# Optimization experiments

Hardware: AMD Instinct MI355X
Metric: run time of the kernel (lower is better)

## Reference

```python
import jax, jax.numpy as jnp
import numpy as np

NE, NR = 200000, 500
D, TRI_H, TET_H = 128, 256, 256
NTRI, NTET = 500000, 200000
B = 8192
E_ET, E_TT, E_ETT = 1500000, 800000, 800000


def _mean_aggregate(src_idx, dst_idx, src, num_dst):
    # scatter-add of gathered messages, then divide by per-dst counts (0 -> 0)
    agg = jax.ops.segment_sum(src[src_idx], dst_idx, num_segments=num_dst)
    cnt = jax.ops.segment_sum(jnp.ones(src_idx.shape[0], dtype=src.dtype), dst_idx, num_segments=num_dst)
    return jnp.where((cnt > 0)[:, None], agg / jnp.maximum(cnt, 1.0)[:, None], 0.0)


def _layernorm(x, w, b, eps=1e-5):
    mu = jnp.mean(x, axis=-1, keepdims=True)
    var = jnp.mean((x - mu) ** 2, axis=-1, keepdims=True)
    return (x - mu) / jnp.sqrt(var + eps) * w + b


def setup_inputs():
    key = jax.random.key(0)
    ks = jax.random.split(key, 24)
    def xav(k, fan_out, fan_in):
        a = np.sqrt(6.0 / (fan_in + fan_out))
        return jax.random.uniform(k, (fan_out, fan_in), jnp.float32, -a, a)
    inp = {
        'entity_emb': xav(ks[0], NE, D),
        'relation_emb': xav(ks[1], NR, D),
        'g2_w1': xav(ks[2], TRI_H, D), 'g2_b1': jnp.zeros((TRI_H,), jnp.float32),
        'g2_w2': xav(ks[3], TRI_H, TRI_H), 'g2_b2': jnp.zeros((TRI_H,), jnp.float32),
        'g3_w1': xav(ks[4], TET_H, TRI_H), 'g3_b1': jnp.zeros((TET_H,), jnp.float32),
        'g3_w2': xav(ks[5], TET_H, TET_H), 'g3_b2': jnp.zeros((TET_H,), jnp.float32),
        'te_w': xav(ks[6], D, TET_H), 'te_b': jnp.zeros((D,), jnp.float32),
        'ln_w': jnp.ones((D,), jnp.float32), 'ln_b': jnp.zeros((D,), jnp.float32),
        'fusion_alpha': jnp.zeros((2,), jnp.float32),
        'gamma': jnp.array([12.0], jnp.float32),
        'triples': jax.random.randint(ks[7], (B, 3), 0, NR, jnp.int64 if jax.config.jax_enable_x64 else jnp.int32),
        'et_index': jax.random.randint(ks[8], (2, E_ET), 0, NE, jnp.int32),
        'tt_index': jax.random.randint(ks[9], (2, E_TT), 0, NTET, jnp.int32),
        'ent_tet_index': jax.random.randint(ks[10], (2, E_ETT), 0, NTET, jnp.int32),
        'num_triangles': NTRI,
        'num_tetras': NTET,
    }
    return inp


def reference(entity_emb, relation_emb, g2_w1, g2_b1, g2_w2, g2_b2,
              g3_w1, g3_b1, g3_w2, g3_b2, te_w, te_b, ln_w, ln_b,
              fusion_alpha, gamma, triples, et_index, tt_index,
              ent_tet_index, num_triangles, num_tetras):
    # gnn2: entity -> triangle  (segment-mean then Linear -> GELU -> Linear)
    tri_agg = _mean_aggregate(et_index[0], et_index[1], entity_emb, num_triangles)
    tri = jax.nn.gelu(tri_agg @ g2_w1.T + g2_b1, approximate=False) @ g2_w2.T + g2_b2
    # gnn3: triangle -> tetra
    tet_agg = _mean_aggregate(tt_index[0], tt_index[1], tri, num_tetras)
    tet = jax.nn.gelu(tet_agg @ g3_w1.T + g3_b1, approximate=False) @ g3_w2.T + g3_b2
    # project tetra -> entity dim, then tetra -> entity mean-aggregate (swapped index rows)
    tet_proj = tet @ te_w.T + te_b
    v_topo = _mean_aggregate(ent_tet_index[1], ent_tet_index[0], tet_proj, entity_emb.shape[0])
    v_topo = _layernorm(v_topo, ln_w, ln_b)
    # learned fusion
    w = jax.nn.softmax(fusion_alpha)
    V = w[0] * entity_emb + w[1] * v_topo
    # TransE scoring: gamma - ||V[h] + R[r] - V[t]||_2
    h, r, t = triples[:, 0], triples[:, 1], triples[:, 2]
    diff = V[h] + relation_emb[r] - V[t]
    return gamma[0] - jnp.sqrt(jnp.sum(diff * diff, axis=-1))
```

## Files before the change

kernel.cpp:

```cpp
#include <hip/hip_runtime.h>
#include <cmath>

#define NE_     200000
#define NR_     500
#define D_      128
#define TRIH_   256
#define TETH_   256
#define NTRI_   500000
#define NTET_   200000
#define B_      8192
#define EET_    1500000
#define ETT_    800000
#define EETT_   800000

#define CAP_V   2048
#define CAP_TP  8192
#define CAP_TRI 12288

#define LCAP_ET  131072
#define LCAP_TT  32768
#define LCAP_ETT 16384

#define COARSEN 8
#define CHUNK   (256 * COARSEN)

#define NBC_V   ((NE_   + CHUNK - 1) / CHUNK)
#define NBC_TP  ((NTET_ + CHUNK - 1) / CHUNK)
#define NBC_TRI ((NTRI_ + CHUNK - 1) / CHUNK)
#define NBF_ET  ((EET_  + CHUNK - 1) / CHUNK)
#define NBF_TT  ((ETT_  + CHUNK - 1) / CHUNK)
#define NBF_ETT ((EETT_ + CHUNK - 1) / CHUNK)
#define MARKB   1024

#define WB_G2W1 0
#define WB_G2W2 32768
#define WB_G3W1 98304
#define WB_G3W2 163840
#define WB_TE   229376


typedef float f32x4 __attribute__((ext_vector_type(4)));
typedef short s16x8 __attribute__((ext_vector_type(8)));

__device__ __forceinline__ float gelu_exact(float v) {
    return 0.5f * v * (1.0f + erff(v * 0.70710678118654752f));
}

__device__ __forceinline__ unsigned short f2bf(float f) {
    unsigned int u = __float_as_uint(f);
    unsigned int r = (u + 0x7fffu + ((u >> 16) & 1u)) >> 16;
    return (unsigned short)r;
}

__device__ __forceinline__ int wave_rank_emit(bool pred, int* lcnt, int lane) {
    unsigned long long mask = __ballot(pred);
    int rank = __popcll(mask & ((1ull << lane) - 1ull));
    int total = __popcll(mask);
    int wb = 0;
    if (lane == 0 && total) wb = atomicAdd(lcnt, total);
    wb = __shfl(wb, 0, 64);
    return pred ? (wb + rank) : -1;
}


__global__ void k_init(int* __restrict__ id_v, int* __restrict__ id_tp,
                       int* __restrict__ id_tri, int* __restrict__ ctr,
                       const float* __restrict__ w1, const float* __restrict__ w2,
                       const float* __restrict__ w3, const float* __restrict__ w4,
                       const float* __restrict__ w5, unsigned short* __restrict__ wb,
                       int* __restrict__ deg_tri, int* __restrict__ deg_tp,
                       int* __restrict__ deg_v) {
    int i = blockIdx.x * blockDim.x + threadIdx.x;
    int st = gridDim.x * blockDim.x;
    for (int x = i; x < NE_; x += st) id_v[x] = -1;
    for (int x = i; x < NTET_; x += st) id_tp[x] = -1;
    for (int x = i; x < NTRI_; x += st) id_tri[x] = -1;
    if (i < 16) ctr[i] = 0;
    for (int x = i; x < 262144; x += st) {
        float f;
        if (x < 32768)       f = w1[x];
        else if (x < 98304)  f = w2[x - 32768];
        else if (x < 163840) f = w3[x - 98304];
        else if (x < 229376) f = w4[x - 163840];
        else                 f = w5[x - 229376];
        wb[x] = f2bf(f);
    }
    for (int x = i; x < CAP_TRI; x += st) deg_tri[x] = 0;
    for (int x = i; x < CAP_TP; x += st) deg_tp[x] = 0;
    for (int x = i; x < CAP_V; x += st) deg_v[x] = 0;
}


__global__ void k_mark_v(const int* __restrict__ triples, int* __restrict__ id_v) {
    int b = blockIdx.x * blockDim.x + threadIdx.x;
    if (b >= B_) return;
    id_v[triples[b * 3 + 0]] = -2;
    id_v[triples[b * 3 + 2]] = -2;
}

__global__ void k_mark_tp(const int* __restrict__ ett, const int* __restrict__ id_v,
                          int* __restrict__ id_tp) {
    int i = blockIdx.x * blockDim.x + threadIdx.x;
    int st = gridDim.x * blockDim.x;
    for (int e = i; e < EETT_; e += st)
        if (id_v[ett[e]] != -1) id_tp[ett[EETT_ + e]] = -2;
}


__device__ void do_compact(int* __restrict__ arr, int n, int* __restrict__ g, int cap,
                           int bid, int* lcnt, int* lbase) {
    if (threadIdx.x == 0) *lcnt = 0;
    __syncthreads();
    const int lane = threadIdx.x & 63;
    const int base = bid * CHUNK;
    int pos[COARSEN];
#pragma unroll
    for (int u = 0; u < COARSEN; ++u) {
        int e = base + u * 256 + threadIdx.x;
        bool pred = (e < n) && (arr[e] == -2);
        pos[u] = wave_rank_emit(pred, lcnt, lane);
    }
    __syncthreads();
    if (threadIdx.x == 0) *lbase = *lcnt ? atomicAdd(g, *lcnt) : 0;
    __syncthreads();
    const int b0 = *lbase;
#pragma unroll
    for (int u = 0; u < COARSEN; ++u) {
        if (pos[u] >= 0) {
            int e = base + u * 256 + threadIdx.x;
            int idx = b0 + pos[u];
            arr[e] = (idx < cap) ? idx : -1;
        }
    }
}

__device__ void do_filter(const int* __restrict__ e0, const int* __restrict__ e1,
                          const int* __restrict__ map0, const int* __restrict__ map1,
                          int n, int2* __restrict__ list, int* __restrict__ nctr, int lcap,
                          int* __restrict__ deg, int bid, int* lcnt, int* lbase) {
    if (threadIdx.x == 0) *lcnt = 0;
    __syncthreads();
    const int lane = threadIdx.x & 63;
    const int base = bid * CHUNK;
    int pos[COARSEN]; int2 val[COARSEN];
#pragma unroll
    for (int u = 0; u < COARSEN; ++u) {
        int e = base + u * 256 + threadIdx.x;
        bool pred = false;
        int m1 = -1, src = -1;
        if (e < n) {
            m1 = map1[e1[e]];
            if (m1 >= 0) {
                src = map0 ? map0[e0[e]] : e0[e];
                pred = (src >= 0);
            }
        }
        pos[u] = wave_rank_emit(pred, lcnt, lane);
        if (pred) { val[u] = make_int2(src, m1); atomicAdd(&deg[m1], 1); }
    }
    __syncthreads();
    if (threadIdx.x == 0) *lbase = *lcnt ? atomicAdd(nctr, *lcnt) : 0;
    __syncthreads();
    const int b0 = *lbase;
#pragma unroll
    for (int u = 0; u < COARSEN; ++u)
        if (pos[u] >= 0 && b0 + pos[u] < lcap) list[b0 + pos[u]] = val[u];
}

__launch_bounds__(256)
__global__ void k_p4(const int* __restrict__ tt, int* __restrict__ id_v,
                     int* __restrict__ id_tp, int* __restrict__ id_tri,
                     int* __restrict__ ctr) {
    __shared__ int lcnt, lbase;
    int bid = blockIdx.x;
    if (bid < NBC_V) { do_compact(id_v, NE_, &ctr[0], CAP_V, bid, &lcnt, &lbase); return; }
    bid -= NBC_V;
    if (bid < NBC_TP) { do_compact(id_tp, NTET_, &ctr[1], CAP_TP, bid, &lcnt, &lbase); return; }
    bid -= NBC_TP;
    int i = bid * 256 + threadIdx.x;
    int st = MARKB * 256;
    for (int e = i; e < ETT_; e += st)
        if (id_tp[tt[ETT_ + e]] != -1) id_tri[tt[e]] = -2;
}

__launch_bounds__(256)
__global__ void k_p5(int* __restrict__ id_tri, const int* __restrict__ ett,
                     const int* __restrict__ id_v, const int* __restrict__ id_tp,
                     int2* __restrict__ list_ett, int* __restrict__ deg_v,
                     int* __restrict__ ctr) {
    __shared__ int lcnt, lbase;
    int bid = blockIdx.x;
    if (bid < NBC_TRI) { do_compact(id_tri, NTRI_, &ctr[2], CAP_TRI, bid, &lcnt, &lbase); return; }
    bid -= NBC_TRI;
    do_filter(ett + EETT_, ett, id_tp, id_v, EETT_, list_ett, &ctr[5], LCAP_ETT,
              deg_v, bid, &lcnt, &lbase);
}

__launch_bounds__(256)
__global__ void k_p6(const int* __restrict__ et, const int* __restrict__ tt,
                     const int* __restrict__ id_tri, const int* __restrict__ id_tp,
                     int2* __restrict__ list_et, int2* __restrict__ list_tt,
                     int* __restrict__ deg_tri, int* __restrict__ deg_tp,
                     int* __restrict__ ctr) {
    __shared__ int lcnt, lbase;
    int bid = blockIdx.x;
    if (bid < NBF_ET) {
        do_filter(et, et + EET_, nullptr, id_tri, EET_, list_et, &ctr[3], LCAP_ET,
                  deg_tri, bid, &lcnt, &lbase);
        return;
    }
    bid -= NBF_ET;
    do_filter(tt, tt + ETT_, id_tri, id_tp, ETT_, list_tt, &ctr[4], LCAP_TT,
              deg_tp, bid, &lcnt, &lbase);
}


__device__ void scan_level(const int* __restrict__ deg, int* __restrict__ start,
                           int* __restrict__ cur, int n) {
    __shared__ int wsum[16];
    const int tid = threadIdx.x;
    const int per = (n + 1023) >> 10;
    const int base = tid * per;
    int s = 0;
    for (int k = 0; k < per; ++k) { int i = base + k; if (i < n) s += deg[i]; }
    const int lane = tid & 63, wid = tid >> 6;
    int v = s;
#pragma unroll
    for (int o = 1; o < 64; o <<= 1) { int t = __shfl_up(v, o, 64); if (lane >= o) v += t; }
    if (lane == 63) wsum[wid] = v;
    __syncthreads();
    if (tid < 16) {
        int w = wsum[tid];
#pragma unroll
        for (int o = 1; o < 16; o <<= 1) { int t = __shfl_up(w, o, 64); if (tid >= o) w += t; }
        wsum[tid] = w;
    }
    __syncthreads();
    int run = v - s + (wid > 0 ? wsum[wid - 1] : 0);
    for (int k = 0; k < per; ++k) {
        int i = base + k;
        if (i < n) { start[i] = run; cur[i] = run; run += deg[i]; }
    }
    if (tid == 0) start[n] = wsum[15];
}

__global__ void k_scan(const int* __restrict__ deg_tri, int* __restrict__ st_tri, int* __restrict__ cu_tri,
                       const int* __restrict__ deg_tp, int* __restrict__ st_tp, int* __restrict__ cu_tp,
                       const int* __restrict__ deg_v, int* __restrict__ st_v, int* __restrict__ cu_v) {
    if (blockIdx.x == 0)      scan_level(deg_tri, st_tri, cu_tri, CAP_TRI);
    else if (blockIdx.x == 1) scan_level(deg_tp, st_tp, cu_tp, CAP_TP);
    else                      scan_level(deg_v, st_v, cu_v, CAP_V);
}

__global__ void k_bucket(const int* __restrict__ ctr,
                         const int2* __restrict__ le, int* __restrict__ cu_tri, int* __restrict__ be,
                         const int2* __restrict__ lt, int* __restrict__ cu_tp, int* __restrict__ btk,
                         const int2* __restrict__ lv, int* __restrict__ cu_v, int* __restrict__ bv) {
    int i = blockIdx.x * blockDim.x + threadIdx.x;
    int st = gridDim.x * blockDim.x;
    int n0 = min(ctr[3], LCAP_ET);
    for (int e = i; e < n0; e += st) {
        int2 p = le[e];
        int slot = atomicAdd(&cu_tri[p.y], 1);
        if (slot < LCAP_ET) be[slot] = p.x;
    }
    int n1 = min(ctr[4], LCAP_TT);
    for (int e = i; e < n1; e += st) {
        int2 p = lt[e];
        int slot = atomicAdd(&cu_tp[p.y], 1);
        if (slot < LCAP_TT) btk[slot] = p.x;
    }
    int n2 = min(ctr[5], LCAP_ETT);
    for (int e = i; e < n2; e += st) {
        int2 p = lv[e];
        int slot = atomicAdd(&cu_v[p.y], 1);
        if (slot < LCAP_ETT) bv[slot] = p.x;
    }
}


__global__ void k_gather_tri(const int* __restrict__ ctr, const int* __restrict__ st,
                             const int* __restrict__ bidx, const float* __restrict__ emb,
                             float* __restrict__ tri_agg) {
    const int c = min(ctr[2], CAP_TRI);
    const int lane = threadIdx.x & 63;
    int row = (blockIdx.x * blockDim.x + threadIdx.x) >> 6;
    const int nw = (gridDim.x * blockDim.x) >> 6;
    for (; row < c; row += nw) {
        int s0 = min(st[row], LCAP_ET), s1 = min(st[row + 1], LCAP_ET);
        float2 acc = make_float2(0.f, 0.f);
        for (int e = s0; e < s1; ++e) {
            unsigned si = (unsigned)bidx[e];
            if (si < NE_) {
                float2 v = ((const float2*)(emb + (size_t)si * 128))[lane];
                acc.x += v.x; acc.y += v.y;
            }
        }
        float inv = (s1 > s0) ? 1.f / (float)(s1 - s0) : 0.f;
        acc.x *= inv; acc.y *= inv;
        ((float2*)(tri_agg + (size_t)row * 128))[lane] = acc;
    }
}


template<int KU>
__device__ __forceinline__ f32x4 tile_mma(const unsigned short* xs, const unsigned short* ws,
                                          int ra, int rb, int fo) {
    f32x4 acc = {0.f, 0.f, 0.f, 0.f};
    const uint4* pa = (const uint4*)xs + ra * KU;
    const uint4* pb = (const uint4*)ws + rb * KU;
    const int sa = ra & 7, sb = rb & 7;
#pragma unroll
    for (int kk = 0; kk < KU / 4; ++kk) {
        s16x8 a = *(const s16x8*)&pa[(kk * 4 + fo) ^ sa];
        s16x8 b = *(const s16x8*)&pb[(kk * 4 + fo) ^ sb];
        acc = __builtin_amdgcn_mfma_f32_16x16x32_bf16(a, b, acc, 0, 0, 0);
    }
    return acc;
}


template<int K, int ACT>
__launch_bounds__(256)
__global__ void k_gemm(const int* __restrict__ ctrp, int ctr_idx, int cap,
                       const float* __restrict__ A,
                       const unsigned short* __restrict__ Wb, const float* __restrict__ bias,
                       float* __restrict__ C, int N) {
    constexpr int KU = K / 8;
    __shared__ __align__(16) unsigned short xs[32 * KU * 8];
    __shared__ __align__(16) unsigned short ws[32 * KU * 8];
    const int c = min(ctrp[ctr_idx], cap);
    const int row0 = blockIdx.x * 32;
    if (row0 >= c) return;
    const int tid = threadIdx.x;
    const int gc0 = blockIdx.y * 32;
#pragma unroll
    for (int it = 0; it < KU / 8; ++it) {
        int u = tid + it * 256;
        int r = u / KU, ku = u % KU;
        int gr = row0 + r;
        s16x8 v;
        if (gr < c) {
            const float* src = &A[(size_t)gr * K + ku * 8];
#pragma unroll
            for (int q = 0; q < 8; ++q) v[q] = (short)f2bf(src[q]);
        } else {
#pragma unroll
            for (int q = 0; q < 8; ++q) v[q] = 0;
        }
        *(s16x8*)&xs[(r * KU + (ku ^ (r & 7))) * 8] = v;
    }
#pragma unroll
    for (int it = 0; it < KU / 8; ++it) {
        int u = tid + it * 256;
        int r = u / KU, ku = u % KU;
        *(uint4*)&ws[(r * KU + (ku ^ (r & 7))) * 8] =
            *(const uint4*)&Wb[(size_t)(gc0 + r) * K + ku * 8];
    }
    __syncthreads();
    const int w = tid >> 6, l = tid & 63;
    const int wr = (w >> 1) * 16, wc = (w & 1) * 16;
    const int fr = l & 15, fo = l >> 4;
    f32x4 acc = tile_mma<KU>(xs, ws, wr + fr, wc + fr, fo);
    const int gcol = gc0 + wc + fr;
    const float bb = bias[gcol];
#pragma unroll
    for (int j = 0; j < 4; ++j) {
        int grow = row0 + wr + fo * 4 + j;
        if (grow < c) {
            float v = acc[j] + bb;
            if (ACT == 1) v = gelu_exact(v);
            C[(size_t)grow * N + gcol] = v;
        }
    }
}


__launch_bounds__(256)
__global__ void k_tet1(const int* __restrict__ ctrp, const int* __restrict__ st,
                       const int* __restrict__ bidx, const float* __restrict__ tri_c,
                       const unsigned short* __restrict__ wb, const float* __restrict__ b1,
                       float* __restrict__ h_tet) {
    __shared__ __align__(16) unsigned short xs[32 * 32 * 8];
    __shared__ __align__(16) unsigned short ws[32 * 32 * 8];
    const int c = min(ctrp[1], CAP_TP);
    const int row0 = blockIdx.x * 32;
    if (row0 >= c) return;
    const int tid = threadIdx.x, lane = tid & 63, wv = tid >> 6;
    for (int rr = wv * 8; rr < wv * 8 + 8; ++rr) {
        int row = row0 + rr;
        float a0 = 0.f, a1 = 0.f, a2 = 0.f, a3 = 0.f;
        int d = 0;
        if (row < c) {
            int s0 = min(st[row], LCAP_TT), s1 = min(st[row + 1], LCAP_TT);
            d = s1 - s0;
            for (int e = s0; e < s1; ++e) {
                unsigned si = (unsigned)bidx[e];
                if (si < CAP_TRI) {
                    float4 v = ((const float4*)(tri_c + (size_t)si * 256))[lane];
                    a0 += v.x; a1 += v.y; a2 += v.z; a3 += v.w;
                }
            }
        }
        float inv = (d > 0) ? 1.f / (float)d : 0.f;
        unsigned lo = (unsigned)f2bf(a0 * inv) | ((unsigned)f2bf(a1 * inv) << 16);
        unsigned hi = (unsigned)f2bf(a2 * inv) | ((unsigned)f2bf(a3 * inv) << 16);
        int col0 = lane * 4;
        int ku = col0 >> 3, off = col0 & 7;
        *(uint2*)&xs[((rr << 5) + (ku ^ (rr & 7))) * 8 + off] = make_uint2(lo, hi);
    }
    const int oc = blockIdx.y;
#pragma unroll
    for (int it = 0; it < 4; ++it) {
        int u = tid + it * 256, r = u >> 5, ku = u & 31;
        *(uint4*)&ws[((r << 5) + (ku ^ (r & 7))) * 8] =
            *(const uint4*)&wb[WB_G3W1 + (size_t)(oc * 32 + r) * 256 + ku * 8];
    }
    __syncthreads();
    const int w = tid >> 6;
    const int wr = (w >> 1) * 16, wc = (w & 1) * 16;
    const int fr = lane & 15, fo = lane >> 4;
    f32x4 acc = tile_mma<32>(xs, ws, wr + fr, wc + fr, fo);
    int col = oc * 32 + wc + fr;
    float bb = b1[col];
#pragma unroll
    for (int j = 0; j < 4; ++j) {
        int grow = row0 + wr + fo * 4 + j;
        if (grow < c) h_tet[(size_t)grow * 256 + col] = gelu_exact(acc[j] + bb);
    }
}


__global__ void k_final(const float* __restrict__ emb, const float* __restrict__ rel,
                        const float* __restrict__ tet_proj, const int* __restrict__ st_v,
                        const int* __restrict__ b_ett, const int* __restrict__ id_v,
                        const float* __restrict__ lnw, const float* __restrict__ lnb,
                        const float* __restrict__ alpha, const float* __restrict__ gamma,
                        const int* __restrict__ triples, float* __restrict__ out) {
    const int lane = threadIdx.x & 63;
    const int b = blockIdx.x * 4 + (threadIdx.x >> 6);
    if (b >= B_) return;
    float a0 = alpha[0], a1 = alpha[1];
    float m = fmaxf(a0, a1);
    float e0 = expf(a0 - m), e1 = expf(a1 - m);
    float w0 = e0 / (e0 + e1), w1 = e1 / (e0 + e1);
    int h = triples[b * 3 + 0];
    int r = triples[b * 3 + 1];
    int t = triples[b * 3 + 2];
    int jh = id_v[h]; jh = (jh >= 0 && jh < CAP_V) ? jh : 0;
    int jt = id_v[t]; jt = (jt >= 0 && jt < CAP_V) ? jt : 0;

    float2 xh = make_float2(0.f, 0.f), xt = make_float2(0.f, 0.f);
    {
        int s0 = min(st_v[jh], LCAP_ETT), s1 = min(st_v[jh + 1], LCAP_ETT);
        for (int e = s0; e < s1; ++e) {
            unsigned si = (unsigned)b_ett[e];
            if (si < CAP_TP) {
                float2 v = ((const float2*)(tet_proj + (size_t)si * 128))[lane];
                xh.x += v.x; xh.y += v.y;
            }
        }
        float inv = (s1 > s0) ? 1.f / (float)(s1 - s0) : 0.f;
        xh.x *= inv; xh.y *= inv;
    }
    {
        int s0 = min(st_v[jt], LCAP_ETT), s1 = min(st_v[jt + 1], LCAP_ETT);
        for (int e = s0; e < s1; ++e) {
            unsigned si = (unsigned)b_ett[e];
            if (si < CAP_TP) {
                float2 v = ((const float2*)(tet_proj + (size_t)si * 128))[lane];
                xt.x += v.x; xt.y += v.y;
            }
        }
        float inv = (s1 > s0) ? 1.f / (float)(s1 - s0) : 0.f;
        xt.x *= inv; xt.y *= inv;
    }
    float sh = xh.x + xh.y, st = xt.x + xt.y;
#pragma unroll
    for (int o = 32; o >= 1; o >>= 1) { sh += __shfl_xor(sh, o, 64); st += __shfl_xor(st, o, 64); }
    float muh = sh * (1.f / 128.f), mut = st * (1.f / 128.f);
    float2 dh = make_float2(xh.x - muh, xh.y - muh);
    float2 dt = make_float2(xt.x - mut, xt.y - mut);
    float vh_ = dh.x * dh.x + dh.y * dh.y, vt_ = dt.x * dt.x + dt.y * dt.y;
#pragma unroll
    for (int o = 32; o >= 1; o >>= 1) { vh_ += __shfl_xor(vh_, o, 64); vt_ += __shfl_xor(vt_, o, 64); }
    float rsh = rsqrtf(vh_ * (1.f / 128.f) + 1e-5f);
    float rst = rsqrtf(vt_ * (1.f / 128.f) + 1e-5f);
    float2 lw = ((const float2*)lnw)[lane];
    float2 lb = ((const float2*)lnb)[lane];
    float2 lnh = make_float2(dh.x * rsh * lw.x + lb.x, dh.y * rsh * lw.y + lb.y);
    float2 lnt = make_float2(dt.x * rst * lw.x + lb.x, dt.y * rst * lw.y + lb.y);
    float2 eh = ((const float2*)emb)[(size_t)h * 64 + lane];
    float2 etv = ((const float2*)emb)[(size_t)t * 64 + lane];
    float2 rr = ((const float2*)rel)[(size_t)r * 64 + lane];
    float dx = (w0 * eh.x + w1 * lnh.x) + rr.x - (w0 * etv.x + w1 * lnt.x);
    float dy = (w0 * eh.y + w1 * lnh.y) + rr.y - (w0 * etv.y + w1 * lnt.y);
    float ss = dx * dx + dy * dy;
#pragma unroll
    for (int o = 32; o >= 1; o >>= 1) ss += __shfl_xor(ss, o, 64);
    if (lane == 0) out[b] = gamma[0] - sqrtf(ss);
}


extern "C" void kernel_launch(void* const* d_in, const int* in_sizes, int n_in,
                              void* d_out, int out_size, void* d_ws, size_t ws_size,
                              hipStream_t stream) {
    const float* entity_emb = (const float*)d_in[0];
    const float* relation_emb = (const float*)d_in[1];
    const float* g2_w1 = (const float*)d_in[2];
    const float* g2_b1 = (const float*)d_in[3];
    const float* g2_w2 = (const float*)d_in[4];
    const float* g2_b2 = (const float*)d_in[5];
    const float* g3_w1 = (const float*)d_in[6];
    const float* g3_b1 = (const float*)d_in[7];
    const float* g3_w2 = (const float*)d_in[8];
    const float* g3_b2 = (const float*)d_in[9];
    const float* te_w = (const float*)d_in[10];
    const float* te_b = (const float*)d_in[11];
    const float* ln_w = (const float*)d_in[12];
    const float* ln_b = (const float*)d_in[13];
    const float* alpha = (const float*)d_in[14];
    const float* gamma = (const float*)d_in[15];
    const int* triples = (const int*)d_in[16];
    const int* et = (const int*)d_in[17];
    const int* tt = (const int*)d_in[18];
    const int* ett = (const int*)d_in[19];
    float* out = (float*)d_out;

    char* base = (char*)d_ws;
    size_t off = 0;
    auto take = [&](size_t bytes) -> void* {
        void* p = base + off;
        off = (off + bytes + 255) & ~(size_t)255;
        return p;
    };
    int* id_v = (int*)take((size_t)NE_ * 4);
    int* id_tp = (int*)take((size_t)NTET_ * 4);
    int* id_tri = (int*)take((size_t)NTRI_ * 4);
    int* ctr = (int*)take(64);
    int* deg_tri = (int*)take((size_t)CAP_TRI * 4);
    int* deg_tp = (int*)take((size_t)CAP_TP * 4);
    int* deg_v = (int*)take((size_t)CAP_V * 4);
    int* st_tri = (int*)take((size_t)(CAP_TRI + 1) * 4);
    int* st_tp = (int*)take((size_t)(CAP_TP + 1) * 4);
    int* st_v = (int*)take((size_t)(CAP_V + 1) * 4);
    int* cu_tri = (int*)take((size_t)CAP_TRI * 4);
    int* cu_tp = (int*)take((size_t)CAP_TP * 4);
    int* cu_v = (int*)take((size_t)CAP_V * 4);
    unsigned short* wb = (unsigned short*)take((size_t)262144 * 2);
    int2* list_et = (int2*)take((size_t)LCAP_ET * 8);
    int2* list_tt = (int2*)take((size_t)LCAP_TT * 8);
    int2* list_ett = (int2*)take((size_t)LCAP_ETT * 8);
    int* b_et = (int*)take((size_t)LCAP_ET * 4);
    int* b_tt = (int*)take((size_t)LCAP_TT * 4);
    int* b_ett = (int*)take((size_t)LCAP_ETT * 4);
    float* tri_agg = (float*)take((size_t)CAP_TRI * D_ * 4);
    float* h_tri = (float*)take((size_t)CAP_TRI * TRIH_ * 4);
    float* tri_c = (float*)take((size_t)CAP_TRI * TRIH_ * 4);
    float* h_tet = (float*)take((size_t)CAP_TP * TETH_ * 4);
    float* y_tet = (float*)take((size_t)CAP_TP * TETH_ * 4);
    float* tet_proj = (float*)take((size_t)CAP_TP * D_ * 4);
    if (off > ws_size) return;

    k_init<<<2048, 256, 0, stream>>>(id_v, id_tp, id_tri, ctr,
                                     g2_w1, g2_w2, g3_w1, g3_w2, te_w, wb,
                                     deg_tri, deg_tp, deg_v);
    k_mark_v<<<(B_ + 255) / 256, 256, 0, stream>>>(triples, id_v);
    k_mark_tp<<<MARKB, 256, 0, stream>>>(ett, id_v, id_tp);
    k_p4<<<NBC_V + NBC_TP + MARKB, 256, 0, stream>>>(tt, id_v, id_tp, id_tri, ctr);
    k_p5<<<NBC_TRI + NBF_ETT, 256, 0, stream>>>(id_tri, ett, id_v, id_tp, list_ett, deg_v, ctr);
    k_p6<<<NBF_ET + NBF_TT, 256, 0, stream>>>(et, tt, id_tri, id_tp, list_et, list_tt,
                                              deg_tri, deg_tp, ctr);
    k_scan<<<3, 1024, 0, stream>>>(deg_tri, st_tri, cu_tri, deg_tp, st_tp, cu_tp,
                                   deg_v, st_v, cu_v);
    k_bucket<<<256, 256, 0, stream>>>(ctr, list_et, cu_tri, b_et,
                                      list_tt, cu_tp, b_tt, list_ett, cu_v, b_ett);
    k_gather_tri<<<2048, 256, 0, stream>>>(ctr, st_tri, b_et, entity_emb, tri_agg);

    dim3 gtri(CAP_TRI / 32, 8);
    k_gemm<128, 1><<<gtri, 256, 0, stream>>>(ctr, 2, CAP_TRI, tri_agg,
                                             wb + WB_G2W1, g2_b1, h_tri, TRIH_);
    k_gemm<256, 0><<<gtri, 256, 0, stream>>>(ctr, 2, CAP_TRI, h_tri,
                                             wb + WB_G2W2, g2_b2, tri_c, TRIH_);
    dim3 gtet(CAP_TP / 32, 8);
    k_tet1<<<gtet, 256, 0, stream>>>(ctr, st_tp, b_tt, tri_c, wb, g3_b1, h_tet);
    k_gemm<256, 0><<<gtet, 256, 0, stream>>>(ctr, 1, CAP_TP, h_tet,
                                             wb + WB_G3W2, g3_b2, y_tet, TETH_);
    dim3 gproj(CAP_TP / 32, 4);
    k_gemm<256, 0><<<gproj, 256, 0, stream>>>(ctr, 1, CAP_TP, y_tet,
                                              wb + WB_TE, te_b, tet_proj, D_);
    k_final<<<(B_ + 3) / 4, 256, 0, stream>>>(entity_emb, relation_emb, tet_proj,
                                              st_v, b_ett, id_v, ln_w, ln_b,
                                              alpha, gamma, triples, out);
}
```

Measured before the change: 149.0 us.

## Store intermediate activations in bf16 and restructure tetra/entity gathers into separate kernels

Intermediate activations (tri_agg, h_tri, tri_c, tet_agg, h_tet, y_tet) are now stored as bf16 instead of fp32. This halves their memory traffic and removes the per-element float-to-bf16 conversion inside the GEMM loads. The GEMM tile widens to 64 output columns per block, with two MFMA accumulators per wave, which halves the grid's y-dimension and reuses each A fragment twice. The fused tet1 aggregation+GEMM is split into a standalone gather followed by the generic GEMM, and the entity mean aggregation moves out of k_final into its own kernel, so head and tail lookups no longer recompute it per triple. The costs are extra bf16 rounding of stored intermediates, two more kernel launches, and GEMM A loads that no longer check the row bound (they read the padded buffer).

After: 133.4 us. 10.4% less time.

```diff
diff --git a/kernel.cpp b/kernel.cpp
--- a/kernel.cpp
+++ b/kernel.cpp
@@ -50,6 +50,10 @@
     unsigned int u = __float_as_uint(f);
     unsigned int r = (u + 0x7fffu + ((u >> 16) & 1u)) >> 16;
     return (unsigned short)r;
+}
+
+__device__ __forceinline__ float bf2f(unsigned int u) {
+    return __uint_as_float(u << 16);
 }
 
 __device__ __forceinline__ int wave_rank_emit(bool pred, int* lcnt, int lane) {
@@ -281,159 +285,146 @@
 
 __global__ void k_gather_tri(const int* __restrict__ ctr, const int* __restrict__ st,
                              const int* __restrict__ bidx, const float* __restrict__ emb,
-                             float* __restrict__ tri_agg) {
+                             unsigned* __restrict__ outb ) {
     const int c = min(ctr[2], CAP_TRI);
     const int lane = threadIdx.x & 63;
     int row = (blockIdx.x * blockDim.x + threadIdx.x) >> 6;
     const int nw = (gridDim.x * blockDim.x) >> 6;
     for (; row < c; row += nw) {
         int s0 = min(st[row], LCAP_ET), s1 = min(st[row + 1], LCAP_ET);
-        float2 acc = make_float2(0.f, 0.f);
+        float ax = 0.f, ay = 0.f;
         for (int e = s0; e < s1; ++e) {
             unsigned si = (unsigned)bidx[e];
             if (si < NE_) {
                 float2 v = ((const float2*)(emb + (size_t)si * 128))[lane];
+                ax += v.x; ay += v.y;
+            }
+        }
+        float inv = (s1 > s0) ? 1.f / (float)(s1 - s0) : 0.f;
+        outb[(size_t)row * 64 + lane] =
+            (unsigned)f2bf(ax * inv) | ((unsigned)f2bf(ay * inv) << 16);
+    }
+}
+
+
+__global__ void k_gather_tt(const int* __restrict__ ctr, const int* __restrict__ st,
+                            const int* __restrict__ bidx, const unsigned short* __restrict__ tri_c,
+                            uint2* __restrict__ outb ) {
+    const int c = min(ctr[1], CAP_TP);
+    const int lane = threadIdx.x & 63;
+    int row = (blockIdx.x * blockDim.x + threadIdx.x) >> 6;
+    const int nw = (gridDim.x * blockDim.x) >> 6;
+    for (; row < c; row += nw) {
+        int s0 = min(st[row], LCAP_TT), s1 = min(st[row + 1], LCAP_TT);
+        float a0 = 0.f, a1 = 0.f, a2 = 0.f, a3 = 0.f;
+        for (int e = s0; e < s1; ++e) {
+            unsigned si = (unsigned)bidx[e];
+            if (si < CAP_TRI) {
+                uint2 p = ((const uint2*)(tri_c + (size_t)si * 256))[lane];
+                a0 += bf2f(p.x & 0xffffu); a1 += bf2f(p.x >> 16);
+                a2 += bf2f(p.y & 0xffffu); a3 += bf2f(p.y >> 16);
+            }
+        }
+        float inv = (s1 > s0) ? 1.f / (float)(s1 - s0) : 0.f;
+        uint2 o;
+        o.x = (unsigned)f2bf(a0 * inv) | ((unsigned)f2bf(a1 * inv) << 16);
+        o.y = (unsigned)f2bf(a2 * inv) | ((unsigned)f2bf(a3 * inv) << 16);
+        outb[(size_t)row * 64 + lane] = o;
+    }
+}
+
+
+__global__ void k_gather_ett(const int* __restrict__ ctr, const int* __restrict__ st,
+                             const int* __restrict__ bidx, const float* __restrict__ tet_proj,
+                             float* __restrict__ v_topo) {
+    const int c = min(ctr[0], CAP_V);
+    const int lane = threadIdx.x & 63;
+    int row = (blockIdx.x * blockDim.x + threadIdx.x) >> 6;
+    const int nw = (gridDim.x * blockDim.x) >> 6;
+    for (; row < c; row += nw) {
+        int s0 = min(st[row], LCAP_ETT), s1 = min(st[row + 1], LCAP_ETT);
+        float2 acc = make_float2(0.f, 0.f);
+        for (int e = s0; e < s1; ++e) {
+            unsigned si = (unsigned)bidx[e];
+            if (si < CAP_TP) {
+                float2 v = ((const float2*)(tet_proj + (size_t)si * 128))[lane];
                 acc.x += v.x; acc.y += v.y;
             }
         }
         float inv = (s1 > s0) ? 1.f / (float)(s1 - s0) : 0.f;
         acc.x *= inv; acc.y *= inv;
-        ((float2*)(tri_agg + (size_t)row * 128))[lane] = acc;
-    }
-}
-
-
-template<int KU>
-__device__ __forceinline__ f32x4 tile_mma(const unsigned short* xs, const unsigned short* ws,
-                                          int ra, int rb, int fo) {
-    f32x4 acc = {0.f, 0.f, 0.f, 0.f};
-    const uint4* pa = (const uint4*)xs + ra * KU;
-    const uint4* pb = (const uint4*)ws + rb * KU;
-    const int sa = ra & 7, sb = rb & 7;
-#pragma unroll
-    for (int kk = 0; kk < KU / 4; ++kk) {
-        s16x8 a = *(const s16x8*)&pa[(kk * 4 + fo) ^ sa];
-        s16x8 b = *(const s16x8*)&pb[(kk * 4 + fo) ^ sb];
-        acc = __builtin_amdgcn_mfma_f32_16x16x32_bf16(a, b, acc, 0, 0, 0);
-    }
-    return acc;
-}
-
-
-template<int K, int ACT>
+        ((float2*)(v_topo + (size_t)row * 128))[lane] = acc;
+    }
+}
+
+
+template<int K, int ACT, bool OBF>
 __launch_bounds__(256)
 __global__ void k_gemm(const int* __restrict__ ctrp, int ctr_idx, int cap,
-                       const float* __restrict__ A,
+                       const unsigned short* __restrict__ A,
                        const unsigned short* __restrict__ Wb, const float* __restrict__ bias,
-                       float* __restrict__ C, int N) {
+                       void* __restrict__ Cv, int N) {
     constexpr int KU = K / 8;
-    __shared__ __align__(16) unsigned short xs[32 * KU * 8];
-    __shared__ __align__(16) unsigned short ws[32 * KU * 8];
+    __shared__ uint4 xs[32 * KU];
+    __shared__ uint4 ws[64 * KU];
     const int c = min(ctrp[ctr_idx], cap);
     const int row0 = blockIdx.x * 32;
     if (row0 >= c) return;
     const int tid = threadIdx.x;
-    const int gc0 = blockIdx.y * 32;
+    const int gc0 = blockIdx.y * 64;
 #pragma unroll
     for (int it = 0; it < KU / 8; ++it) {
         int u = tid + it * 256;
         int r = u / KU, ku = u % KU;
-        int gr = row0 + r;
-        s16x8 v;
-        if (gr < c) {
-            const float* src = &A[(size_t)gr * K + ku * 8];
-#pragma unroll
-            for (int q = 0; q < 8; ++q) v[q] = (short)f2bf(src[q]);
-        } else {
-#pragma unroll
-            for (int q = 0; q < 8; ++q) v[q] = 0;
-        }
-        *(s16x8*)&xs[(r * KU + (ku ^ (r & 7))) * 8] = v;
-    }
-#pragma unroll
-    for (int it = 0; it < KU / 8; ++it) {
+        xs[r * KU + (ku ^ (r & 7))] = *(const uint4*)&A[(size_t)(row0 + r) * K + ku * 8];
+    }
+#pragma unroll
+    for (int it = 0; it < KU / 4; ++it) {
         int u = tid + it * 256;
         int r = u / KU, ku = u % KU;
-        *(uint4*)&ws[(r * KU + (ku ^ (r & 7))) * 8] =
-            *(const uint4*)&Wb[(size_t)(gc0 + r) * K + ku * 8];
-    }
-    __syncthreads();
+        ws[r * KU + (ku ^ (r & 7))] = *(const uint4*)&Wb[(size_t)(gc0 + r) * K + ku * 8];
+    }
+    __syncthreads();
+
     const int w = tid >> 6, l = tid & 63;
-    const int wr = (w >> 1) * 16, wc = (w & 1) * 16;
+    const int wr = (w >> 1) * 16, wc0 = (w & 1) * 32;
     const int fr = l & 15, fo = l >> 4;
-    f32x4 acc = tile_mma<KU>(xs, ws, wr + fr, wc + fr, fo);
-    const int gcol = gc0 + wc + fr;
-    const float bb = bias[gcol];
+    const int ra = wr + fr, rb0 = wc0 + fr, rb1 = wc0 + 16 + fr;
+    f32x4 acc0 = {0.f, 0.f, 0.f, 0.f}, acc1 = {0.f, 0.f, 0.f, 0.f};
+    const uint4* pa = xs + ra * KU;   const int sa = ra & 7;
+    const uint4* pb0 = ws + rb0 * KU; const int sb0 = rb0 & 7;
+    const uint4* pb1 = ws + rb1 * KU; const int sb1 = rb1 & 7;
+#pragma unroll
+    for (int kk = 0; kk < KU / 4; ++kk) {
+        s16x8 a = *(const s16x8*)&pa[(kk * 4 + fo) ^ sa];
+        s16x8 b0 = *(const s16x8*)&pb0[(kk * 4 + fo) ^ sb0];
+        s16x8 b1 = *(const s16x8*)&pb1[(kk * 4 + fo) ^ sb1];
+        acc0 = __builtin_amdgcn_mfma_f32_16x16x32_bf16(a, b0, acc0, 0, 0, 0);
+        acc1 = __builtin_amdgcn_mfma_f32_16x16x32_bf16(a, b1, acc1, 0, 0, 0);
+    }
+    const int col0 = gc0 + wc0 + fr, col1 = col0 + 16;
+    const float bb0 = bias[col0], bb1 = bias[col1];
 #pragma unroll
     for (int j = 0; j < 4; ++j) {
         int grow = row0 + wr + fo * 4 + j;
         if (grow < c) {
-            float v = acc[j] + bb;
-            if (ACT == 1) v = gelu_exact(v);
-            C[(size_t)grow * N + gcol] = v;
-        }
-    }
-}
-
-
-__launch_bounds__(256)
-__global__ void k_tet1(const int* __restrict__ ctrp, const int* __restrict__ st,
-                       const int* __restrict__ bidx, const float* __restrict__ tri_c,
-                       const unsigned short* __restrict__ wb, const float* __restrict__ b1,
-                       float* __restrict__ h_tet) {
-    __shared__ __align__(16) unsigned short xs[32 * 32 * 8];
-    __shared__ __align__(16) unsigned short ws[32 * 32 * 8];
-    const int c = min(ctrp[1], CAP_TP);
-    const int row0 = blockIdx.x * 32;
-    if (row0 >= c) return;
-    const int tid = threadIdx.x, lane = tid & 63, wv = tid >> 6;
-    for (int rr = wv * 8; rr < wv * 8 + 8; ++rr) {
-        int row = row0 + rr;
-        float a0 = 0.f, a1 = 0.f, a2 = 0.f, a3 = 0.f;
-        int d = 0;
-        if (row < c) {
-            int s0 = min(st[row], LCAP_TT), s1 = min(st[row + 1], LCAP_TT);
-            d = s1 - s0;
-            for (int e = s0; e < s1; ++e) {
-                unsigned si = (unsigned)bidx[e];
-                if (si < CAP_TRI) {
-                    float4 v = ((const float4*)(tri_c + (size_t)si * 256))[lane];
-                    a0 += v.x; a1 += v.y; a2 += v.z; a3 += v.w;
-                }
+            float v0 = acc0[j] + bb0;
+            float v1 = acc1[j] + bb1;
+            if (ACT == 1) { v0 = gelu_exact(v0); v1 = gelu_exact(v1); }
+            if (OBF) {
+                ((unsigned short*)Cv)[(size_t)grow * N + col0] = f2bf(v0);
+                ((unsigned short*)Cv)[(size_t)grow * N + col1] = f2bf(v1);
+            } else {
+                ((float*)Cv)[(size_t)grow * N + col0] = v0;
+                ((float*)Cv)[(size_t)grow * N + col1] = v1;
             }
         }
-        float inv = (d > 0) ? 1.f / (float)d : 0.f;
-        unsigned lo = (unsigned)f2bf(a0 * inv) | ((unsigned)f2bf(a1 * inv) << 16);
-        unsigned hi = (unsigned)f2bf(a2 * inv) | ((unsigned)f2bf(a3 * inv) << 16);
-        int col0 = lane * 4;
-        int ku = col0 >> 3, off = col0 & 7;
-        *(uint2*)&xs[((rr << 5) + (ku ^ (rr & 7))) * 8 + off] = make_uint2(lo, hi);
-    }
-    const int oc = blockIdx.y;
-#pragma unroll
-    for (int it = 0; it < 4; ++it) {
-        int u = tid + it * 256, r = u >> 5, ku = u & 31;
-        *(uint4*)&ws[((r << 5) + (ku ^ (r & 7))) * 8] =
-            *(const uint4*)&wb[WB_G3W1 + (size_t)(oc * 32 + r) * 256 + ku * 8];
-    }
-    __syncthreads();
-    const int w = tid >> 6;
-    const int wr = (w >> 1) * 16, wc = (w & 1) * 16;
-    const int fr = lane & 15, fo = lane >> 4;
-    f32x4 acc = tile_mma<32>(xs, ws, wr + fr, wc + fr, fo);
-    int col = oc * 32 + wc + fr;
-    float bb = b1[col];
-#pragma unroll
-    for (int j = 0; j < 4; ++j) {
-        int grow = row0 + wr + fo * 4 + j;
-        if (grow < c) h_tet[(size_t)grow * 256 + col] = gelu_exact(acc[j] + bb);
     }
 }
 
 
 __global__ void k_final(const float* __restrict__ emb, const float* __restrict__ rel,
-                        const float* __restrict__ tet_proj, const int* __restrict__ st_v,
-                        const int* __restrict__ b_ett, const int* __restrict__ id_v,
+                        const float* __restrict__ v_topo, const int* __restrict__ id_v,
                         const float* __restrict__ lnw, const float* __restrict__ lnb,
                         const float* __restrict__ alpha, const float* __restrict__ gamma,
                         const int* __restrict__ triples, float* __restrict__ out) {
@@ -449,32 +440,9 @@
     int t = triples[b * 3 + 2];
     int jh = id_v[h]; jh = (jh >= 0 && jh < CAP_V) ? jh : 0;
     int jt = id_v[t]; jt = (jt >= 0 && jt < CAP_V) ? jt : 0;
-
-    float2 xh = make_float2(0.f, 0.f), xt = make_float2(0.f, 0.f);
-    {
-        int s0 = min(st_v[jh], LCAP_ETT), s1 = min(st_v[jh + 1], LCAP_ETT);
-        for (int e = s0; e < s1; ++e) {
-            unsigned si = (unsigned)b_ett[e];
-            if (si < CAP_TP) {
-                float2 v = ((const float2*)(tet_proj + (size_t)si * 128))[lane];
-                xh.x += v.x; xh.y += v.y;
-            }
-        }
-        float inv = (s1 > s0) ? 1.f / (float)(s1 - s0) : 0.f;
-        xh.x *= inv; xh.y *= inv;
-    }
-    {
-        int s0 = min(st_v[jt], LCAP_ETT), s1 = min(st_v[jt + 1], LCAP_ETT);
-        for (int e = s0; e < s1; ++e) {
-            unsigned si = (unsigned)b_ett[e];
-            if (si < CAP_TP) {
-                float2 v = ((const float2*)(tet_proj + (size_t)si * 128))[lane];
-                xt.x += v.x; xt.y += v.y;
-            }
-        }
-        float inv = (s1 > s0) ? 1.f / (float)(s1 - s0) : 0.f;
-        xt.x *= inv; xt.y *= inv;
-    }
+    const float2* vt2 = (const float2*)v_topo;
+    float2 xh = vt2[(size_t)jh * 64 + lane];
+    float2 xt = vt2[(size_t)jt * 64 + lane];
     float sh = xh.x + xh.y, st = xt.x + xt.y;
 #pragma unroll
     for (int o = 32; o >= 1; o >>= 1) { sh += __shfl_xor(sh, o, 64); st += __shfl_xor(st, o, 64); }
@@ -554,12 +522,14 @@
     int* b_et = (int*)take((size_t)LCAP_ET * 4);
     int* b_tt = (int*)take((size_t)LCAP_TT * 4);
     int* b_ett = (int*)take((size_t)LCAP_ETT * 4);
-    float* tri_agg = (float*)take((size_t)CAP_TRI * D_ * 4);
-    float* h_tri = (float*)take((size_t)CAP_TRI * TRIH_ * 4);
-    float* tri_c = (float*)take((size_t)CAP_TRI * TRIH_ * 4);
-    float* h_tet = (float*)take((size_t)CAP_TP * TETH_ * 4);
-    float* y_tet = (float*)take((size_t)CAP_TP * TETH_ * 4);
+    unsigned short* tri_agg = (unsigned short*)take((size_t)CAP_TRI * D_ * 2);
+    unsigned short* h_tri = (unsigned short*)take((size_t)CAP_TRI * TRIH_ * 2);
+    unsigned short* tri_c = (unsigned short*)take((size_t)CAP_TRI * TRIH_ * 2);
+    unsigned short* tet_agg = (unsigned short*)take((size_t)CAP_TP * TRIH_ * 2);
+    unsigned short* h_tet = (unsigned short*)take((size_t)CAP_TP * TETH_ * 2);
+    unsigned short* y_tet = (unsigned short*)take((size_t)CAP_TP * TETH_ * 2);
     float* tet_proj = (float*)take((size_t)CAP_TP * D_ * 4);
+    float* v_topo = (float*)take((size_t)CAP_V * D_ * 4);
     if (off > ws_size) return;
 
     k_init<<<2048, 256, 0, stream>>>(id_v, id_tp, id_tri, ctr,
@@ -575,21 +545,24 @@
                                    deg_v, st_v, cu_v);
     k_bucket<<<256, 256, 0, stream>>>(ctr, list_et, cu_tri, b_et,
                                       list_tt, cu_tp, b_tt, list_ett, cu_v, b_ett);
-    k_gather_tri<<<2048, 256, 0, stream>>>(ctr, st_tri, b_et, entity_emb, tri_agg);
-
-    dim3 gtri(CAP_TRI / 32, 8);
-    k_gemm<128, 1><<<gtri, 256, 0, stream>>>(ctr, 2, CAP_TRI, tri_agg,
-                                             wb + WB_G2W1, g2_b1, h_tri, TRIH_);
-    k_gemm<256, 0><<<gtri, 256, 0, stream>>>(ctr, 2, CAP_TRI, h_tri,
-                                             wb + WB_G2W2, g2_b2, tri_c, TRIH_);
-    dim3 gtet(CAP_TP / 32, 8);
-    k_tet1<<<gtet, 256, 0, stream>>>(ctr, st_tp, b_tt, tri_c, wb, g3_b1, h_tet);
-    k_gemm<256, 0><<<gtet, 256, 0, stream>>>(ctr, 1, CAP_TP, h_tet,
-                                             wb + WB_G3W2, g3_b2, y_tet, TETH_);
-    dim3 gproj(CAP_TP / 32, 4);
-    k_gemm<256, 0><<<gproj, 256, 0, stream>>>(ctr, 1, CAP_TP, y_tet,
-                                              wb + WB_TE, te_b, tet_proj, D_);
-    k_final<<<(B_ + 3) / 4, 256, 0, stream>>>(entity_emb, relation_emb, tet_proj,
-                                              st_v, b_ett, id_v, ln_w, ln_b,
-                                              alpha, gamma, triples, out);
-}
+    k_gather_tri<<<2048, 256, 0, stream>>>(ctr, st_tri, b_et, entity_emb, (unsigned*)tri_agg);
+
+    dim3 gtri(CAP_TRI / 32, TRIH_ / 64);
+    k_gemm<128, 1, true><<<gtri, 256, 0, stream>>>(ctr, 2, CAP_TRI, tri_agg,
+                                                   wb + WB_G2W1, g2_b1, h_tri, TRIH_);
+    k_gemm<256, 0, true><<<gtri, 256, 0, stream>>>(ctr, 2, CAP_TRI, h_tri,
+                                                   wb + WB_G2W2, g2_b2, tri_c, TRIH_);
+    k_gather_tt<<<256, 256, 0, stream>>>(ctr, st_tp, b_tt, tri_c, (uint2*)tet_agg);
+
+    dim3 gtet(CAP_TP / 32, TETH_ / 64);
+    k_gemm<256, 1, true><<<gtet, 256, 0, stream>>>(ctr, 1, CAP_TP, tet_agg,
+                                                   wb + WB_G3W1, g3_b1, h_tet, TETH_);
+    k_gemm<256, 0, true><<<gtet, 256, 0, stream>>>(ctr, 1, CAP_TP, h_tet,
+                                                   wb + WB_G3W2, g3_b2, y_tet, TETH_);
+    dim3 gproj(CAP_TP / 32, D_ / 64);
+    k_gemm<256, 0, false><<<gproj, 256, 0, stream>>>(ctr, 1, CAP_TP, y_tet,
+                                                     wb + WB_TE, te_b, tet_proj, D_);
+    k_gather_ett<<<128, 256, 0, stream>>>(ctr, st_v, b_ett, tet_proj, v_topo);
+    k_final<<<(B_ + 3) / 4, 256, 0, stream>>>(entity_emb, relation_emb, v_topo, id_v,
+                                              ln_w, ln_b, alpha, gamma, triples, out);
+}
```
